# Optimization experiments

Measured on AMD Instinct MI355X. Metric: run time of the kernel, lower is better.

Reference implementation:

```python
import jax, jax.numpy as jnp
import numpy as np

DIM = 256
HEADS = 8
BALL = 128          # ball_size m
DIMENSIONALITY = 3
HIDDEN = 4 * DIM    # mlp_ratio * dim
HEAD_DIM = DIM // HEADS
EPS = 1e-6


def setup_inputs() -> dict:
    key = jax.random.key(0)
    ks = jax.random.split(key, 16)
    N = 131072
    s = lambda *sh: 1.0 / np.sqrt(sh[-1])
    inp = {
        "x": jax.random.normal(ks[0], (N, DIM), jnp.float32),
        "pos": jax.random.normal(ks[1], (N, DIMENSIONALITY), jnp.float32),
        "num_batches": 8,
        # BallMSA params
        "qkv_w": jax.random.normal(ks[2], (3 * DIM, DIM), jnp.float32) * s(DIM),
        "qkv_b": jnp.zeros((3 * DIM,), jnp.float32),
        "proj_w": jax.random.normal(ks[3], (DIM, DIM), jnp.float32) * s(DIM),
        "proj_b": jnp.zeros((DIM,), jnp.float32),
        "pe_w": jax.random.normal(ks[4], (DIM, DIMENSIONALITY), jnp.float32) * s(DIMENSIONALITY),
        "pe_b": jnp.zeros((DIM,), jnp.float32),
        "sigma_att": -1.0 + 0.01 * jax.random.normal(ks[5], (1, HEADS, 1, 1), jnp.float32),
        # norms
        "norm1_w": jnp.ones((DIM,), jnp.float32),
        "norm2_w": jnp.ones((DIM,), jnp.float32),
        # SwiGLU MLP
        "w1_w": jax.random.normal(ks[6], (HIDDEN, DIM), jnp.float32) * s(DIM),
        "w1_b": jnp.zeros((HIDDEN,), jnp.float32),
        "w2_w": jax.random.normal(ks[7], (HIDDEN, DIM), jnp.float32) * s(DIM),
        "w2_b": jnp.zeros((HIDDEN,), jnp.float32),
        "w3_w": jax.random.normal(ks[8], (DIM, HIDDEN), jnp.float32) * s(HIDDEN),
        "w3_b": jnp.zeros((DIM,), jnp.float32),
    }
    return inp


def _rmsnorm(x, w):
    return x * jax.lax.rsqrt(jnp.mean(x * x, axis=-1, keepdims=True) + EPS) * w


def _ball_msa(x, pos, qkv_w, qkv_b, proj_w, proj_b, pe_w, pe_b, sigma_att):
    N = x.shape[0]
    n = N // BALL
    p = pos.reshape(n, BALL, DIMENSIONALITY)
    # relative position wrt ball center (eq. 9), torch.no_grad in original
    rel = jax.lax.stop_gradient((p - p.mean(axis=1, keepdims=True)).reshape(N, DIMENSIONALITY))
    x = x + rel @ pe_w.T + pe_b
    # qkv: last dim laid out as (H E K) with K innermost
    qkv = (x @ qkv_w.T + qkv_b).reshape(n, BALL, HEADS, HEAD_DIM, 3)
    q = jnp.transpose(qkv[..., 0], (0, 2, 1, 3))  # n H m E
    k = jnp.transpose(qkv[..., 1], (0, 2, 1, 3))
    v = jnp.transpose(qkv[..., 2], (0, 2, 1, 3))
    # distance-based bias (eq. 10), torch.no_grad in original
    d = jnp.sqrt(jnp.sum((p[:, :, None, :] - p[:, None, :, :]) ** 2, axis=-1))  # n m m
    bias = jax.lax.stop_gradient(sigma_att[0]) * jax.lax.stop_gradient(d)[:, None, :, :]  # n H m m
    scores = jnp.einsum('nhme,nhke->nhmk', q, k) / np.sqrt(HEAD_DIM) + bias
    attn = jax.nn.softmax(scores, axis=-1)
    out = jnp.einsum('nhmk,nhke->nhme', attn, v)
    out = jnp.transpose(out, (0, 2, 1, 3)).reshape(N, DIM)  # (n m) (H E)
    return out @ proj_w.T + proj_b


def reference(x, pos, num_batches, qkv_w, qkv_b, proj_w, proj_b, pe_w, pe_b,
              sigma_att, norm1_w, norm2_w, w1_w, w1_b, w2_w, w2_b, w3_w, w3_b):
    # pre-norm block: x + BMSA(norm1(x)); x + SwiGLU(norm2(x))
    x = x + _ball_msa(_rmsnorm(x, norm1_w), pos, qkv_w, qkv_b, proj_w, proj_b,
                      pe_w, pe_b, sigma_att)
    h = _rmsnorm(x, norm2_w)
    gate = jax.nn.silu(h @ w1_w.T + w1_b)
    val = h @ w2_w.T + w2_b
    return x + (gate * val) @ w3_w.T + w3_b
```

## Files before the change

kernel.cpp:

```cpp
#include <hip/hip_runtime.h>

typedef __bf16 bf16x8 __attribute__((ext_vector_type(8)));
typedef float f32x4 __attribute__((ext_vector_type(4)));

__device__ __forceinline__ float b2f(unsigned short u) {
    union { unsigned int i; float f; } v; v.i = ((unsigned int)u) << 16; return v.f;
}
__device__ __forceinline__ unsigned short f2b(float f) {
    union { float f; unsigned int i; } v; v.f = f;
    unsigned int r = (v.i + 0x7fffu + ((v.i >> 16) & 1u)) >> 16;
    return (unsigned short)r;
}

__device__ __forceinline__ void gload16(const void* g, void* l) {
    __builtin_amdgcn_global_load_lds(
        (const __attribute__((address_space(1))) unsigned int*)g,
        (__attribute__((address_space(3))) unsigned int*)l,
        16, 0, 0);
}

__device__ __forceinline__ void xcd_map(int bid, int nx, int ny, int& bx, int& by) {
    if ((nx & 7) == 0) {
        int xcd = bid & 7;
        int s   = bid >> 3;
        int xl  = s / ny;
        by = s - xl * ny;
        bx = xcd * (nx >> 3) + xl;
    } else {
        bx = bid / ny;
        by = bid - bx * ny;
    }
}

__global__ __launch_bounds__(256)
void k_cvt5(const float* __restrict__ s0, const float* __restrict__ s1,
            const float* __restrict__ s2, const float* __restrict__ s3,
            const float* __restrict__ s4, unsigned short* __restrict__ dst)
{
    size_t gid = ((size_t)blockIdx.x * 256 + threadIdx.x) * 4;
    const float* src; size_t off;
    if      (gid < 196608) { src = s0; off = 0; }
    else if (gid < 262144) { src = s1; off = 196608; }
    else if (gid < 524288) { src = s2; off = 262144; }
    else if (gid < 786432) { src = s3; off = 524288; }
    else                   { src = s4; off = 786432; }
    float4 v = *(const float4*)(src + (gid - off));
    uint2 pk;
    pk.x = (unsigned int)f2b(v.x) | ((unsigned int)f2b(v.y) << 16);
    pk.y = (unsigned int)f2b(v.z) | ((unsigned int)f2b(v.w) << 16);
    *(uint2*)(dst + gid) = pk;
}

__global__ __launch_bounds__(256)
void k_norm1_pe(const float* __restrict__ x,
                const float* __restrict__ pos,
                const float* __restrict__ n1w,
                const float* __restrict__ pew,
                const float* __restrict__ peb,
                unsigned short* __restrict__ out)
{
    __shared__ float spw0[256], spw1[256], spw2[256], speb[256], snw[256];
    __shared__ float px[128], py[128], pz[128];
    __shared__ float mean[3];
    const int tid = threadIdx.x;
    const int ball = blockIdx.x;

    spw0[tid] = pew[tid*3+0]; spw1[tid] = pew[tid*3+1]; spw2[tid] = pew[tid*3+2];
    speb[tid] = peb[tid];     snw[tid]  = n1w[tid];
    if (tid < 128) {
        const float* pp = pos + (size_t)(ball*128 + tid)*3;
        px[tid] = pp[0]; py[tid] = pp[1]; pz[tid] = pp[2];
    }
    __syncthreads();
    if (tid < 3) {
        const float* arr = (tid==0) ? px : (tid==1) ? py : pz;
        float s = 0.f;
        for (int i = 0; i < 128; ++i) s += arr[i];
        mean[tid] = s * (1.0f/128.0f);
    }
    __syncthreads();

    const int wave = tid >> 6, lane = tid & 63;
    const float m0 = mean[0], m1 = mean[1], m2 = mean[2];
    for (int tok = wave; tok < 128; tok += 4) {
        size_t row = (size_t)(ball*128 + tok);
        float4 xv = *(const float4*)(x + row*256 + lane*4);
        float xf[4] = { xv.x, xv.y, xv.z, xv.w };
        float ss = xf[0]*xf[0] + xf[1]*xf[1] + xf[2]*xf[2] + xf[3]*xf[3];
        #pragma unroll
        for (int off = 1; off < 64; off <<= 1) ss += __shfl_xor(ss, off);
        float rstd = rsqrtf(ss * (1.0f/256.0f) + 1e-6f);
        float r0 = px[tok] - m0, r1 = py[tok] - m1, r2 = pz[tok] - m2;
        unsigned short o[4];
        #pragma unroll
        for (int k = 0; k < 4; ++k) {
            int j = lane*4 + k;
            float hv = xf[k] * rstd * snw[j];
            o[k] = f2b(hv + r0*spw0[j] + r1*spw1[j] + r2*spw2[j] + speb[j]);
        }
        uint2 pk;
        pk.x = (unsigned int)o[0] | ((unsigned int)o[1] << 16);
        pk.y = (unsigned int)o[2] | ((unsigned int)o[3] << 16);
        *(uint2*)(out + row*256 + lane*4) = pk;
    }
}

__global__ __launch_bounds__(256)
void k_rmsnorm(const float* __restrict__ x,
               const float* __restrict__ w,
               unsigned short* __restrict__ out)
{
    const int lane = threadIdx.x & 63;
    const size_t token = (size_t)blockIdx.x*4 + (threadIdx.x >> 6);
    float4 xv = *(const float4*)(x + token*256 + lane*4);
    float xf[4] = { xv.x, xv.y, xv.z, xv.w };
    float ss = xf[0]*xf[0] + xf[1]*xf[1] + xf[2]*xf[2] + xf[3]*xf[3];
    #pragma unroll
    for (int off = 1; off < 64; off <<= 1) ss += __shfl_xor(ss, off);
    float rstd = rsqrtf(ss * (1.0f/256.0f) + 1e-6f);
    float4 wv = *(const float4*)(w + lane*4);
    unsigned short o[4] = { f2b(xf[0]*rstd*wv.x), f2b(xf[1]*rstd*wv.y),
                            f2b(xf[2]*rstd*wv.z), f2b(xf[3]*rstd*wv.w) };
    uint2 pk;
    pk.x = (unsigned int)o[0] | ((unsigned int)o[1] << 16);
    pk.y = (unsigned int)o[2] | ((unsigned int)o[3] << 16);
    *(uint2*)(out + token*256 + lane*4) = pk;
}

__device__ __forceinline__ void gemm_mainloop_bt(
    const unsigned short* __restrict__ A, const unsigned short* __restrict__ B,
    int K, int m0, int n0, int tid,
    unsigned short* sA, unsigned short* sB, f32x4 (&acc)[4][4])
{
    const int lane = tid & 63, lane16 = lane & 15, quad = lane >> 4;
    const int wave = tid >> 6;
    const int wm = (wave >> 1) * 64, wn = (wave & 1) * 64;
    const int srow = wave * 32 + (lane >> 2);
    const int scol = (lane & 3) * 8;
    const unsigned short* pA = A + (size_t)(m0 + srow) * K + scol;
    const unsigned short* pB = B + (size_t)(n0 + srow) * K + scol;
    const size_t row16 = (size_t)16 * K;
    unsigned short* lA = sA + wave * 1024;
    unsigned short* lB = sB + wave * 1024;

    for (int k0 = 0; k0 < K; k0 += 32) {
        __syncthreads();
        gload16(pA + k0,         lA);
        gload16(pA + row16 + k0, lA + 512);
        gload16(pB + k0,         lB);
        gload16(pB + row16 + k0, lB + 512);
        __syncthreads();
        bf16x8 af[4], bfr[4];
        #pragma unroll
        for (int i = 0; i < 4; ++i) af[i]  = *(const bf16x8*)&sA[(wm + i*16 + lane16)*32 + quad*8];
        #pragma unroll
        for (int j = 0; j < 4; ++j) bfr[j] = *(const bf16x8*)&sB[(wn + j*16 + lane16)*32 + quad*8];
        #pragma unroll
        for (int i = 0; i < 4; ++i)
            #pragma unroll
            for (int j = 0; j < 4; ++j)
                acc[i][j] = __builtin_amdgcn_mfma_f32_16x16x32_bf16(af[i], bfr[j], acc[i][j], 0, 0, 0);
    }
}

__global__ __launch_bounds__(256, 2)
void k_gemm_bias(const unsigned short* __restrict__ A,
                 const unsigned short* __restrict__ B,
                 const float* __restrict__ bias,
                 const float* residual,
                 void* C, int K, int Ncols, int outBf16, int ny)
{
    __shared__ __align__(16) unsigned short sA[128*32];
    __shared__ __align__(16) unsigned short sB[128*32];
    const int tid = threadIdx.x;
    int bx, by;
    xcd_map(blockIdx.x, gridDim.x / ny, ny, bx, by);
    const int m0 = bx * 128, n0 = by * 128;
    f32x4 zero = {0.f, 0.f, 0.f, 0.f};
    f32x4 acc[4][4];
    #pragma unroll
    for (int i = 0; i < 4; ++i)
        #pragma unroll
        for (int j = 0; j < 4; ++j) acc[i][j] = zero;

    gemm_mainloop_bt(A, B, K, m0, n0, tid, sA, sB, acc);

    const int lane = tid & 63, lane16 = lane & 15, quad = lane >> 4;
    const int wave = tid >> 6, wm = (wave >> 1) * 64, wn = (wave & 1) * 64;
    #pragma unroll
    for (int i = 0; i < 4; ++i)
        #pragma unroll
        for (int j = 0; j < 4; ++j) {
            int n = n0 + wn + j*16 + lane16;
            float bj = bias[n];
            #pragma unroll
            for (int r = 0; r < 4; ++r) {
                int m = m0 + wm + i*16 + quad*4 + r;
                size_t idx = (size_t)m * Ncols + n;
                float v = acc[i][j][r] + bj;
                if (residual) v += residual[idx];
                if (outBf16) ((unsigned short*)C)[idx] = f2b(v);
                else         ((float*)C)[idx] = v;
            }
        }
}

__global__ __launch_bounds__(256, 3)
void k_gemm_swiglu(const unsigned short* __restrict__ A,
                   const unsigned short* __restrict__ B1,
                   const unsigned short* __restrict__ B2,
                   const float* __restrict__ b1,
                   const float* __restrict__ b2,
                   unsigned short* __restrict__ C, int K, int ny)
{
    __shared__ __align__(16) unsigned short sA[128*32];
    __shared__ __align__(16) unsigned short sB1[64*32];
    __shared__ __align__(16) unsigned short sB2[64*32];
    const int tid = threadIdx.x;
    int bx, by;
    xcd_map(blockIdx.x, gridDim.x / ny, ny, bx, by);
    const int m0 = bx * 128, n0 = by * 64;
    const int lane = tid & 63, lane16 = lane & 15, quad = lane >> 4;
    const int wave = tid >> 6;
    const int wm = (wave >> 1) * 64, wn = (wave & 1) * 32;
    const int srowA = wave * 32 + (lane >> 2);
    const int srowB = wave * 16 + (lane >> 2);
    const int scol  = (lane & 3) * 8;
    const unsigned short* pA  = A  + (size_t)(m0 + srowA) * K + scol;
    const unsigned short* pB1 = B1 + (size_t)(n0 + srowB) * K + scol;
    const unsigned short* pB2 = B2 + (size_t)(n0 + srowB) * K + scol;
    const size_t row16 = (size_t)16 * K;
    unsigned short* lA  = sA  + wave * 1024;
    unsigned short* lB1 = sB1 + wave * 512;
    unsigned short* lB2 = sB2 + wave * 512;

    f32x4 zero = {0.f, 0.f, 0.f, 0.f};
    f32x4 accg[4][2], accv[4][2];
    #pragma unroll
    for (int i = 0; i < 4; ++i)
        #pragma unroll
        for (int j = 0; j < 2; ++j) { accg[i][j] = zero; accv[i][j] = zero; }

    for (int k0 = 0; k0 < K; k0 += 32) {
        __syncthreads();
        gload16(pA + k0,         lA);
        gload16(pA + row16 + k0, lA + 512);
        gload16(pB1 + k0,        lB1);
        gload16(pB2 + k0,        lB2);
        __syncthreads();
        bf16x8 af[4], bg[2], bv[2];
        #pragma unroll
        for (int i = 0; i < 4; ++i) af[i] = *(const bf16x8*)&sA[(wm + i*16 + lane16)*32 + quad*8];
        #pragma unroll
        for (int j = 0; j < 2; ++j) {
            bg[j] = *(const bf16x8*)&sB1[(wn + j*16 + lane16)*32 + quad*8];
            bv[j] = *(const bf16x8*)&sB2[(wn + j*16 + lane16)*32 + quad*8];
        }
        #pragma unroll
        for (int i = 0; i < 4; ++i)
            #pragma unroll
            for (int j = 0; j < 2; ++j) {
                accg[i][j] = __builtin_amdgcn_mfma_f32_16x16x32_bf16(af[i], bg[j], accg[i][j], 0, 0, 0);
                accv[i][j] = __builtin_amdgcn_mfma_f32_16x16x32_bf16(af[i], bv[j], accv[i][j], 0, 0, 0);
            }
    }

    #pragma unroll
    for (int i = 0; i < 4; ++i)
        #pragma unroll
        for (int j = 0; j < 2; ++j) {
            int n = n0 + wn + j*16 + lane16;
            float bjg = b1[n], bjv = b2[n];
            #pragma unroll
            for (int r = 0; r < 4; ++r) {
                int m = m0 + wm + i*16 + quad*4 + r;
                float g  = accg[i][j][r] + bjg;
                float vv = accv[i][j][r] + bjv;
                float sg = 1.0f / (1.0f + __expf(-g));
                C[(size_t)m * 1024 + n] = f2b(g * sg * vv);
            }
        }
}

__global__ __launch_bounds__(256, 2)
void k_attn(const unsigned short* __restrict__ qkv,
            const float* __restrict__ pos,
            const float* __restrict__ sigma,
            unsigned short* __restrict__ out)
{
    __shared__ __align__(16) unsigned short Qs[128*40];
    __shared__ __align__(16) unsigned short Ks[128*40];
    __shared__ __align__(16) unsigned short Vt[32*136];
    __shared__ __align__(16) unsigned short Ps[128*136];
    __shared__ float px[128], py[128], pz[128];

    int ball, h;
    xcd_map(blockIdx.x, gridDim.x >> 3, 8, ball, h);
    const int tid  = threadIdx.x;

    {
        int tok = tid >> 1;
        int e0  = (tid & 1) * 16;
        const unsigned short* rowp = qkv + (size_t)(ball*128 + tok)*768 + h*96 + e0*3;
        unsigned short u[48];
        #pragma unroll
        for (int c = 0; c < 6; ++c) *(uint4*)&u[c*8] = *(const uint4*)(rowp + c*8);
        #pragma unroll
        for (int e = 0; e < 16; ++e) {
            Qs[tok*40 + e0 + e]    = u[e*3 + 0];
            Ks[tok*40 + e0 + e]    = u[e*3 + 1];
            Vt[(e0 + e)*136 + tok] = u[e*3 + 2];
        }
    }
    if (tid < 128) {
        const float* pp = pos + (size_t)(ball*128 + tid)*3;
        px[tid] = pp[0]; py[tid] = pp[1]; pz[tid] = pp[2];
    }
    __syncthreads();

    const int wave = tid >> 6, lane = tid & 63, lane16 = lane & 15, quad = lane >> 4;
    const float sig = sigma[h];
    const float scale = 0.17677669529663687f;
    f32x4 zero = {0.f, 0.f, 0.f, 0.f};

    f32x4 s[2][8];
    {
        bf16x8 a[2];
        #pragma unroll
        for (int i = 0; i < 2; ++i)
            a[i] = *(const bf16x8*)&Qs[(wave*32 + i*16 + lane16)*40 + quad*8];
        #pragma unroll
        for (int j = 0; j < 8; ++j) {
            bf16x8 b = *(const bf16x8*)&Ks[(j*16 + lane16)*40 + quad*8];
            #pragma unroll
            for (int i = 0; i < 2; ++i)
                s[i][j] = __builtin_amdgcn_mfma_f32_16x16x32_bf16(a[i], b, zero, 0, 0, 0);
        }
    }

    float pnx[8], pny[8], pnz[8];
    #pragma unroll
    for (int j = 0; j < 8; ++j) {
        int n = j*16 + lane16;
        pnx[j] = px[n]; pny[j] = py[n]; pnz[j] = pz[n];
    }
    float l[2][4];
    #pragma unroll
    for (int i = 0; i < 2; ++i)
        #pragma unroll
        for (int r = 0; r < 4; ++r) {
            int m = wave*32 + i*16 + quad*4 + r;
            float pmx = px[m], pmy = py[m], pmz = pz[m];
            float sv[8];
            float mx = -1e30f;
            #pragma unroll
            for (int j = 0; j < 8; ++j) {
                float dx = pmx - pnx[j], dy = pmy - pny[j], dz = pmz - pnz[j];
                float d = sqrtf(dx*dx + dy*dy + dz*dz);
                float val = s[i][j][r] * scale + sig * d;
                sv[j] = val;
                mx = fmaxf(mx, val);
            }
            #pragma unroll
            for (int off = 1; off < 16; off <<= 1) mx = fmaxf(mx, __shfl_xor(mx, off, 16));
            float sum = 0.f;
            #pragma unroll
            for (int j = 0; j < 8; ++j) {
                float p = __expf(sv[j] - mx);
                sum += p;
                Ps[(size_t)m*136 + j*16 + lane16] = f2b(p);
            }
            #pragma unroll
            for (int off = 1; off < 16; off <<= 1) sum += __shfl_xor(sum, off, 16);
            l[i][r] = sum;
        }
    __syncthreads();

    f32x4 o[2][2];
    #pragma unroll
    for (int i = 0; i < 2; ++i)
        #pragma unroll
        for (int nf = 0; nf < 2; ++nf) o[i][nf] = zero;
    #pragma unroll
    for (int c = 0; c < 4; ++c) {
        bf16x8 pa[2];
        #pragma unroll
        for (int i = 0; i < 2; ++i)
            pa[i] = *(const bf16x8*)&Ps[(wave*32 + i*16 + lane16)*136 + c*32 + quad*8];
        #pragma unroll
        for (int nf = 0; nf < 2; ++nf) {
            bf16x8 vb = *(const bf16x8*)&Vt[(nf*16 + lane16)*136 + c*32 + quad*8];
            #pragma unroll
            for (int i = 0; i < 2; ++i)
                o[i][nf] = __builtin_amdgcn_mfma_f32_16x16x32_bf16(pa[i], vb, o[i][nf], 0, 0, 0);
        }
    }

    #pragma unroll
    for (int i = 0; i < 2; ++i)
        #pragma unroll
        for (int nf = 0; nf < 2; ++nf)
            #pragma unroll
            for (int r = 0; r < 4; ++r) {
                int m = wave*32 + i*16 + quad*4 + r;
                out[(size_t)(ball*128 + m)*256 + h*32 + nf*16 + lane16] = f2b(o[i][nf][r] / l[i][r]);
            }
}

extern "C" void kernel_launch(void* const* d_in, const int* in_sizes, int n_in,
                              void* d_out, int out_size, void* d_ws, size_t ws_size,
                              hipStream_t stream)
{
    const float* x      = (const float*)d_in[0];
    const float* pos    = (const float*)d_in[1];
    const float* qkv_w  = (const float*)d_in[3];
    const float* qkv_b  = (const float*)d_in[4];
    const float* proj_w = (const float*)d_in[5];
    const float* proj_b = (const float*)d_in[6];
    const float* pe_w   = (const float*)d_in[7];
    const float* pe_b   = (const float*)d_in[8];
    const float* sigma  = (const float*)d_in[9];
    const float* n1w    = (const float*)d_in[10];
    const float* n2w    = (const float*)d_in[11];
    const float* w1w    = (const float*)d_in[12];
    const float* w1b    = (const float*)d_in[13];
    const float* w2w    = (const float*)d_in[14];
    const float* w2b    = (const float*)d_in[15];
    const float* w3w    = (const float*)d_in[16];
    const float* w3b    = (const float*)d_in[17];

    const int N = in_sizes[0] / 256;
    float* out = (float*)d_out;

    unsigned short* wb      = (unsigned short*)d_ws;
    unsigned short* qkv_wb  = wb;
    unsigned short* proj_wb = wb + 196608;
    unsigned short* w1wb    = wb + 262144;
    unsigned short* w2wb    = wb + 524288;
    unsigned short* w3wb    = wb + 786432;

    int C = 1;
    while (2097152 + (size_t)(N / C) * 2560 > ws_size && C < 256) C <<= 1;
    const int R = N / C;
    unsigned short* regA = wb + 1048576;
    unsigned short* regB = regA + (size_t)R * 1024;

    k_cvt5<<<1024, 256, 0, stream>>>(qkv_w, proj_w, w1w, w2w, w3w, wb);

    for (int c = 0; c < C; ++c) {
        const size_t row0 = (size_t)c * R;
        const float* x_c   = x   + row0 * 256;
        const float* pos_c = pos + row0 * 3;
        float* out_c = out + row0 * 256;
        const int nball_c = R / 128;
        const int nx = R / 128;

        k_norm1_pe<<<nball_c, 256, 0, stream>>>(x_c, pos_c, n1w, pe_w, pe_b, regB);
        k_gemm_bias<<<nx * 6, 256, 0, stream>>>(regB, qkv_wb, qkv_b, nullptr, regA, 256, 768, 1, 6);
        k_attn<<<nball_c * 8, 256, 0, stream>>>(regA, pos_c, sigma, regB);
        k_gemm_bias<<<nx * 2, 256, 0, stream>>>(regB, proj_wb, proj_b, x_c, out_c, 256, 256, 0, 2);
        k_rmsnorm<<<R/4, 256, 0, stream>>>(out_c, n2w, regB);
        k_gemm_swiglu<<<nx * 16, 256, 0, stream>>>(regB, w1wb, w2wb, w1b, w2b, regA, 256, 16);
        k_gemm_bias<<<nx * 2, 256, 0, stream>>>(regA, w3wb, w3b, out_c, out_c, 1024, 256, 0, 2);
    }
}
```

Baseline: 1.076 ms.

## Double-buffer LDS tiles and use conflict-free fragment layout in GEMM kernels

Both GEMM mainloops now keep two LDS stages. The next K-slice is prefetched with global_load_lds while MFMAs run on the current one, which drops one barrier per iteration. The loader's thread-to-row mapping is also changed so that each lane's bf16x8 fragment sits contiguously in LDS (lane*8). This gives bank-conflict-free, linear fragment reads. In exchange LDS use doubles, and launch bounds for the bias GEMM are raised to 3 blocks per CU, which may limit registers.

```diff
diff --git a/kernel.cpp b/kernel.cpp
--- a/kernel.cpp
+++ b/kernel.cpp
@@ -132,46 +132,56 @@
     int K, int m0, int n0, int tid,
     unsigned short* sA, unsigned short* sB, f32x4 (&acc)[4][4])
 {
-    const int lane = tid & 63, lane16 = lane & 15, quad = lane >> 4;
+    const int lane = tid & 63;
     const int wave = tid >> 6;
-    const int wm = (wave >> 1) * 64, wn = (wave & 1) * 64;
-    const int srow = wave * 32 + (lane >> 2);
-    const int scol = (lane & 3) * 8;
+    const int srow = wave * 32 + (lane & 15);
+    const int scol = (lane >> 4) * 8;
     const unsigned short* pA = A + (size_t)(m0 + srow) * K + scol;
     const unsigned short* pB = B + (size_t)(n0 + srow) * K + scol;
     const size_t row16 = (size_t)16 * K;
-    unsigned short* lA = sA + wave * 1024;
-    unsigned short* lB = sB + wave * 1024;
-
+    const int stO = wave * 1024;
+    const int aBase = (wave >> 1) * 2048 + lane * 8;
+    const int bBase = (wave & 1) * 2048 + lane * 8;
+
+    gload16(pA, sA + stO);  gload16(pA + row16, sA + stO + 512);
+    gload16(pB, sB + stO);  gload16(pB + row16, sB + stO + 512);
+    __syncthreads();
+
+    int cur = 0;
     for (int k0 = 0; k0 < K; k0 += 32) {
-        __syncthreads();
-        gload16(pA + k0,         lA);
-        gload16(pA + row16 + k0, lA + 512);
-        gload16(pB + k0,         lB);
-        gload16(pB + row16 + k0, lB + 512);
-        __syncthreads();
+        if (k0 + 32 < K) {
+            const int nxt = (cur ^ 1) * 4096 + stO;
+            gload16(pA + k0 + 32,         sA + nxt);
+            gload16(pA + row16 + k0 + 32, sA + nxt + 512);
+            gload16(pB + k0 + 32,         sB + nxt);
+            gload16(pB + row16 + k0 + 32, sB + nxt + 512);
+        }
+        const unsigned short* cA = sA + cur * 4096;
+        const unsigned short* cB = sB + cur * 4096;
         bf16x8 af[4], bfr[4];
         #pragma unroll
-        for (int i = 0; i < 4; ++i) af[i]  = *(const bf16x8*)&sA[(wm + i*16 + lane16)*32 + quad*8];
-        #pragma unroll
-        for (int j = 0; j < 4; ++j) bfr[j] = *(const bf16x8*)&sB[(wn + j*16 + lane16)*32 + quad*8];
+        for (int i = 0; i < 4; ++i) af[i]  = *(const bf16x8*)&cA[aBase + i*512];
+        #pragma unroll
+        for (int j = 0; j < 4; ++j) bfr[j] = *(const bf16x8*)&cB[bBase + j*512];
         #pragma unroll
         for (int i = 0; i < 4; ++i)
             #pragma unroll
             for (int j = 0; j < 4; ++j)
                 acc[i][j] = __builtin_amdgcn_mfma_f32_16x16x32_bf16(af[i], bfr[j], acc[i][j], 0, 0, 0);
-    }
-}
-
-__global__ __launch_bounds__(256, 2)
+        __syncthreads();
+        cur ^= 1;
+    }
+}
+
+__global__ __launch_bounds__(256, 3)
 void k_gemm_bias(const unsigned short* __restrict__ A,
                  const unsigned short* __restrict__ B,
                  const float* __restrict__ bias,
                  const float* residual,
                  void* C, int K, int Ncols, int outBf16, int ny)
 {
-    __shared__ __align__(16) unsigned short sA[128*32];
-    __shared__ __align__(16) unsigned short sB[128*32];
+    __shared__ __align__(16) unsigned short sA[2*4096];
+    __shared__ __align__(16) unsigned short sB[2*4096];
     const int tid = threadIdx.x;
     int bx, by;
     xcd_map(blockIdx.x, gridDim.x / ny, ny, bx, by);
@@ -213,9 +223,9 @@
                    const float* __restrict__ b2,
                    unsigned short* __restrict__ C, int K, int ny)
 {
-    __shared__ __align__(16) unsigned short sA[128*32];
-    __shared__ __align__(16) unsigned short sB1[64*32];
-    __shared__ __align__(16) unsigned short sB2[64*32];
+    __shared__ __align__(16) unsigned short sA[2*4096];
+    __shared__ __align__(16) unsigned short sB1[2*2048];
+    __shared__ __align__(16) unsigned short sB2[2*2048];
     const int tid = threadIdx.x;
     int bx, by;
     xcd_map(blockIdx.x, gridDim.x / ny, ny, bx, by);
@@ -223,16 +233,17 @@
     const int lane = tid & 63, lane16 = lane & 15, quad = lane >> 4;
     const int wave = tid >> 6;
     const int wm = (wave >> 1) * 64, wn = (wave & 1) * 32;
-    const int srowA = wave * 32 + (lane >> 2);
-    const int srowB = wave * 16 + (lane >> 2);
-    const int scol  = (lane & 3) * 8;
+    const int srowA = wave * 32 + (lane & 15);
+    const int srowB = wave * 16 + (lane & 15);
+    const int scol  = (lane >> 4) * 8;
     const unsigned short* pA  = A  + (size_t)(m0 + srowA) * K + scol;
     const unsigned short* pB1 = B1 + (size_t)(n0 + srowB) * K + scol;
     const unsigned short* pB2 = B2 + (size_t)(n0 + srowB) * K + scol;
     const size_t row16 = (size_t)16 * K;
-    unsigned short* lA  = sA  + wave * 1024;
-    unsigned short* lB1 = sB1 + wave * 512;
-    unsigned short* lB2 = sB2 + wave * 512;
+    const int stA = wave * 1024;
+    const int stB = wave * 512;
+    const int aBase = (wave >> 1) * 2048 + lane * 8;
+    const int bBase = (wave & 1) * 1024 + lane * 8;
 
     f32x4 zero = {0.f, 0.f, 0.f, 0.f};
     f32x4 accg[4][2], accv[4][2];
@@ -241,20 +252,29 @@
         #pragma unroll
         for (int j = 0; j < 2; ++j) { accg[i][j] = zero; accv[i][j] = zero; }
 
+    gload16(pA, sA + stA);  gload16(pA + row16, sA + stA + 512);
+    gload16(pB1, sB1 + stB);
+    gload16(pB2, sB2 + stB);
+    __syncthreads();
+
+    int cur = 0;
     for (int k0 = 0; k0 < K; k0 += 32) {
-        __syncthreads();
-        gload16(pA + k0,         lA);
-        gload16(pA + row16 + k0, lA + 512);
-        gload16(pB1 + k0,        lB1);
-        gload16(pB2 + k0,        lB2);
-        __syncthreads();
+        if (k0 + 32 < K) {
+            gload16(pA + k0 + 32,         sA  + (cur^1)*4096 + stA);
+            gload16(pA + row16 + k0 + 32, sA  + (cur^1)*4096 + stA + 512);
+            gload16(pB1 + k0 + 32,        sB1 + (cur^1)*2048 + stB);
+            gload16(pB2 + k0 + 32,        sB2 + (cur^1)*2048 + stB);
+        }
+        const unsigned short* cA  = sA  + cur * 4096;
+        const unsigned short* cB1 = sB1 + cur * 2048;
+        const unsigned short* cB2 = sB2 + cur * 2048;
         bf16x8 af[4], bg[2], bv[2];
         #pragma unroll
-        for (int i = 0; i < 4; ++i) af[i] = *(const bf16x8*)&sA[(wm + i*16 + lane16)*32 + quad*8];
+        for (int i = 0; i < 4; ++i) af[i] = *(const bf16x8*)&cA[aBase + i*512];
         #pragma unroll
         for (int j = 0; j < 2; ++j) {
-            bg[j] = *(const bf16x8*)&sB1[(wn + j*16 + lane16)*32 + quad*8];
-            bv[j] = *(const bf16x8*)&sB2[(wn + j*16 + lane16)*32 + quad*8];
+            bg[j] = *(const bf16x8*)&cB1[bBase + j*512];
+            bv[j] = *(const bf16x8*)&cB2[bBase + j*512];
         }
         #pragma unroll
         for (int i = 0; i < 4; ++i)
@@ -263,6 +283,8 @@
                 accg[i][j] = __builtin_amdgcn_mfma_f32_16x16x32_bf16(af[i], bg[j], accg[i][j], 0, 0, 0);
                 accv[i][j] = __builtin_amdgcn_mfma_f32_16x16x32_bf16(af[i], bv[j], accv[i][j], 0, 0, 0);
             }
+        __syncthreads();
+        cur ^= 1;
     }
 
     #pragma unroll
```

After: 1.217 ms. +13.1%, slower.
